# Optimization experiments

Hardware: AMD Instinct MI355X
Metric: run time of the kernel (lower is better)

## Reference

```python
import jax, jax.numpy as jnp
import numpy as np

B, H, W, C, NH, WS, SS = 32, 56, 56, 192, 6, 7, 3
N = WS * WS
HD = C // NH
NW = (H // WS) * (W // WS)
HID = 4 * C
RPB_SIZE = (2 * WS - 1) * (2 * WS - 1)


def _rel_index():
    coords = np.stack(np.meshgrid(np.arange(WS), np.arange(WS), indexing='ij')).reshape(2, -1)
    rel = (coords[:, :, None] - coords[:, None, :]).transpose(1, 2, 0)
    rel[..., 0] += WS - 1
    rel[..., 1] += WS - 1
    rel[..., 0] *= 2 * WS - 1
    return rel.sum(-1)  # (N, N) int

REL_IDX = jnp.asarray(_rel_index())


def _swin_attn_mask():
    # standard Swin shifted-window mask: -100 for cross-region pairs
    img = np.zeros((H, W))
    cnt = 0
    for hs in (slice(0, -WS), slice(-WS, -SS), slice(-SS, None)):
        for ws_ in (slice(0, -WS), slice(-WS, -SS), slice(-SS, None)):
            img[hs, ws_] = cnt
            cnt += 1
    win = img.reshape(H // WS, WS, W // WS, WS).transpose(0, 2, 1, 3).reshape(-1, N)
    diff = win[:, None, :] - win[:, :, None]
    return np.where(diff != 0, -100.0, 0.0).astype(np.float32)  # (NW, N, N)


def _ln(t, g, b, eps=1e-5):
    mu = t.mean(-1, keepdims=True)
    v = ((t - mu) ** 2).mean(-1, keepdims=True)
    return (t - mu) * jax.lax.rsqrt(v + eps) * g + b


def setup_inputs() -> dict:
    key = jax.random.key(0)
    ks = jax.random.split(key, 12)
    s = 0.02
    return {
        'x': jax.random.normal(ks[0], (B, H * W, C), jnp.float32),
        'attn_mask': jnp.asarray(_swin_attn_mask()),
        'ln1_g': jnp.ones((C,), jnp.float32),
        'ln1_b': jnp.zeros((C,), jnp.float32),
        'qkv_w': jax.random.normal(ks[1], (C, 3 * C), jnp.float32) * s,
        'qkv_b': jnp.zeros((3 * C,), jnp.float32),
        'rpb': jax.random.normal(ks[2], (RPB_SIZE, NH), jnp.float32) * s,
        'proj_w': jax.random.normal(ks[3], (C, C), jnp.float32) * s,
        'proj_b': jnp.zeros((C,), jnp.float32),
        'ln2_g': jnp.ones((C,), jnp.float32),
        'ln2_b': jnp.zeros((C,), jnp.float32),
        'fc1_w': jax.random.normal(ks[4], (C, HID), jnp.float32) * s,
        'fc1_b': jnp.zeros((HID,), jnp.float32),
        'fc2_w': jax.random.normal(ks[5], (HID, C), jnp.float32) * s,
        'fc2_b': jnp.zeros((C,), jnp.float32),
    }


def reference(x, attn_mask, ln1_g, ln1_b, qkv_w, qkv_b, rpb, proj_w, proj_b,
              ln2_g, ln2_b, fc1_w, fc1_b, fc2_w, fc2_b):
    shortcut = x
    h = _ln(x, ln1_g, ln1_b).reshape(B, H, W, C)
    # cyclic shift
    h = jnp.roll(h, (-SS, -SS), axis=(1, 2))
    # window partition -> (B*NW, N, C)
    h = h.reshape(B, H // WS, WS, W // WS, WS, C).transpose(0, 1, 3, 2, 4, 5).reshape(B * NW, N, C)
    qkv = (h @ qkv_w + qkv_b).reshape(B * NW, N, 3, NH, HD).transpose(2, 0, 3, 1, 4)
    q, k, v = qkv[0] * (HD ** -0.5), qkv[1], qkv[2]
    attn = jnp.einsum('bhnd,bhmd->bhnm', q, k)  # (B*NW, NH, N, N)
    bias = rpb[REL_IDX].transpose(2, 0, 1)      # (NH, N, N)
    attn = attn + bias[None]
    attn = attn.reshape(B, NW, NH, N, N) + attn_mask[None, :, None]
    attn = jax.nn.softmax(attn.reshape(B * NW, NH, N, N), axis=-1)
    o = jnp.einsum('bhnm,bhmd->bhnd', attn, v).transpose(0, 2, 1, 3).reshape(B * NW, N, C)
    o = o @ proj_w + proj_b
    # window reverse + reverse shift
    o = o.reshape(B, H // WS, W // WS, WS, WS, C).transpose(0, 1, 3, 2, 4, 5).reshape(B, H, W, C)
    o = jnp.roll(o, (SS, SS), axis=(1, 2)).reshape(B, H * W, C)
    x1 = shortcut + o
    m = _ln(x1, ln2_g, ln2_b)
    m = jax.nn.gelu(m @ fc1_w + fc1_b, approximate=False) @ fc2_w + fc2_b
    return x1 + m
```

## Files before the change

kernel.cpp:

```cpp
#include <hip/hip_runtime.h>
#include <hip/hip_bf16.h>

typedef __hip_bfloat16 bf16;
typedef __attribute__((ext_vector_type(8))) short short8;
typedef __attribute__((ext_vector_type(4))) float f32x4;
typedef __attribute__((ext_vector_type(4))) unsigned short ushort4_t;

#define TOK 100352
#define NWIN 2048
#define CC 192
#define NHEAD 6
#define NT 49

__device__ __forceinline__ float bf2f(bf16 v) { return __bfloat162float(v); }
__device__ __forceinline__ bf16 f2bf(float v) { return __float2bfloat16(v); }
__device__ __forceinline__ float b2f_bits(unsigned short u) {
    return __uint_as_float(((unsigned)u) << 16);
}

__device__ __forceinline__ float ldin(const void* p, size_t i, int f) {
    return f ? ((const float*)p)[i] : bf2f(((const bf16*)p)[i]);
}
__device__ __forceinline__ void stc(bf16* p, float v) { *p = f2bf(v); }
__device__ __forceinline__ void stc(float* p, float v) { *p = v; }
__device__ __forceinline__ float ldc(const bf16* p) { return bf2f(*p); }
__device__ __forceinline__ float ldc(const float* p) { return *p; }

__device__ __forceinline__ void gl_lds16(const bf16* g, bf16* l) {
    __builtin_amdgcn_global_load_lds(
        (const __attribute__((address_space(1))) unsigned int*)g,
        (__attribute__((address_space(3))) unsigned int*)l, 16, 0, 0);
}

__global__ void dtype_probe_kernel(const void* xraw, int* flag) {
    const unsigned short* u = (const unsigned short*)xraw;
    int lane = threadIdx.x & 63;
    int weird = 0;
    for (int i = lane; i < 4096; i += 64) {
        unsigned int bits = ((unsigned int)u[2 * i]) << 16;
        float v = __uint_as_float(bits);
        if (!(fabsf(v) <= 1e10f)) weird++;
    }
    #pragma unroll
    for (int off = 32; off > 0; off >>= 1) weird += __shfl_xor(weird, off, 64);
    if (lane == 0) *flag = (weird > 256) ? 1 : 0;
}

__global__ void transpose_kernel(const void* __restrict__ in, bf16* __restrict__ out,
                                 int K, int N, const int* __restrict__ flag) {
    int f = *flag;
    int idx = blockIdx.x * 256 + threadIdx.x;
    if (idx >= K * N) return;
    int nn = idx / K, kk = idx % K;
    out[idx] = f2bf(ldin(in, (size_t)kk * N + nn, f));
}

__global__ __launch_bounds__(256) void comb_kernel(
    const void* __restrict__ rpb, const void* __restrict__ mask,
    bf16* __restrict__ comb, const int* __restrict__ flag) {
    int f = *flag;
    int idx = blockIdx.x * 256 + threadIdx.x;
    int m = idx & 63;
    int n = (idx >> 6) & 63;
    int hw = idx >> 12;
    int head = hw % NHEAD, wi = hw / NHEAD;
    float v;
    if (n < NT && m < NT) {
        int nr = n / 7, nc = n % 7, mr = m / 7, mc = m % 7;
        int ridx = (nr - mr + 6) * 13 + (nc - mc + 6);
        v = ldin(rpb, (size_t)ridx * NHEAD + head, f)
          + ldin(mask, (size_t)wi * NT * NT + n * NT + m, f);
    } else {
        v = -1e30f;
    }
    comb[idx] = f2bf(v);
}

__global__ __launch_bounds__(256) void ln1_window_kernel(
    const void* __restrict__ x, const void* __restrict__ g, const void* __restrict__ b,
    bf16* __restrict__ hwin, const int* __restrict__ flag) {
    int f = *flag;
    int wave = threadIdx.x >> 6, lane = threadIdx.x & 63;
    int t = blockIdx.x * 4 + wave;
    int bidx = t / (64 * NT);
    int r = t % (64 * NT);
    int wi = r / NT, n = r % NT;
    int wr = wi >> 3, wc = wi & 7;
    int nr = n / 7, nc = n % 7;
    int si = wr * 7 + nr, sj = wc * 7 + nc;
    int oi = si + 3; if (oi >= 56) oi -= 56;
    int oj = sj + 3; if (oj >= 56) oj -= 56;
    size_t src = ((size_t)bidx * 3136 + oi * 56 + oj) * CC;
    float v0 = ldin(x, src + lane, f);
    float v1 = ldin(x, src + lane + 64, f);
    float v2 = ldin(x, src + lane + 128, f);
    float s = v0 + v1 + v2;
    float sq = v0 * v0 + v1 * v1 + v2 * v2;
    #pragma unroll
    for (int off = 32; off > 0; off >>= 1) {
        s  += __shfl_xor(s, off, 64);
        sq += __shfl_xor(sq, off, 64);
    }
    float mu = s * (1.f / 192.f);
    float var = fmaxf(sq * (1.f / 192.f) - mu * mu, 0.f);
    float rs = rsqrtf(var + 1e-5f);
    bf16* dst = hwin + (size_t)t * CC;
    dst[lane]       = f2bf((v0 - mu) * rs * ldin(g, lane, f)       + ldin(b, lane, f));
    dst[lane + 64]  = f2bf((v1 - mu) * rs * ldin(g, lane + 64, f)  + ldin(b, lane + 64, f));
    dst[lane + 128] = f2bf((v2 - mu) * rs * ldin(g, lane + 128, f) + ldin(b, lane + 128, f));
}

template <int EPI, typename CT>
__global__ __launch_bounds__(256, 4) void gemm_kernel(
    const bf16* __restrict__ A, const bf16* __restrict__ Wt,
    const void* __restrict__ bias, CT* __restrict__ C,
    const CT* __restrict__ resid, int M, int K, int Nc, const int* __restrict__ flag) {
    int f = *flag;
    __shared__ __align__(16) bf16 sb[2][(128 + 64) * 32];
    int bn = blockIdx.x, bm = blockIdx.y;
    int tid = threadIdx.x;
    int wave = tid >> 6, lane = tid & 63;
    int quad = lane >> 4, l16 = lane & 15;

    const bf16* ag[2];
    #pragma unroll
    for (int j = 0; j < 2; j++) {
        int k = wave * 2 + j;
        ag[j] = A + (size_t)(bm * 128 + k * 16 + (lane >> 2)) * K + (lane & 3) * 8;
    }
    const bf16* bg = Wt + (size_t)(bn * 64 + wave * 16 + (lane >> 2)) * K + (lane & 3) * 8;

    f32x4 acc[2][4];
    #pragma unroll
    for (int i = 0; i < 2; i++)
        #pragma unroll
        for (int j = 0; j < 4; j++)
            acc[i][j][0] = acc[i][j][1] = acc[i][j][2] = acc[i][j][3] = 0.f;

    const int nt = K >> 5;

    #pragma unroll
    for (int j = 0; j < 2; j++)
        gl_lds16(ag[j], &sb[0][(wave * 2 + j) * 512]);
    gl_lds16(bg, &sb[0][4096 + wave * 512]);
    __syncthreads();

    int ct = 0;
    for (int t = 0; t < nt; t++) {
        if (t + 1 < nt) {
            #pragma unroll
            for (int j = 0; j < 2; j++) {
                ag[j] += 32;
                gl_lds16(ag[j], &sb[ct ^ 1][(wave * 2 + j) * 512]);
            }
            bg += 32;
            gl_lds16(bg, &sb[ct ^ 1][4096 + wave * 512]);
        }
        const bf16* sA = &sb[ct][0];
        const bf16* sB = &sb[ct][4096];
        short8 av[2], bv[4];
        #pragma unroll
        for (int tm = 0; tm < 2; tm++)
            av[tm] = *(const short8*)(&sA[(wave * 32 + tm * 16 + l16) * 32 + quad * 8]);
        #pragma unroll
        for (int tn = 0; tn < 4; tn++)
            bv[tn] = *(const short8*)(&sB[(tn * 16 + l16) * 32 + quad * 8]);
        #pragma unroll
        for (int tm = 0; tm < 2; tm++)
            #pragma unroll
            for (int tn = 0; tn < 4; tn++)
                acc[tm][tn] = __builtin_amdgcn_mfma_f32_16x16x32_bf16(av[tm], bv[tn], acc[tm][tn], 0, 0, 0);
        if (t + 1 < nt) {
            __syncthreads();
            ct ^= 1;
        }
    }

    #pragma unroll
    for (int tm = 0; tm < 2; tm++)
        #pragma unroll
        for (int tn = 0; tn < 4; tn++) {
            int col = bn * 64 + tn * 16 + l16;
            float bvs = ldin(bias, col, f);
            #pragma unroll
            for (int r = 0; r < 4; r++) {
                int row = bm * 128 + wave * 32 + tm * 16 + quad * 4 + r;
                float v = acc[tm][tn][r] + bvs;
                if (EPI == 1) v = 0.5f * v * (1.0f + erff(v * 0.70710678118654752f));
                if (EPI == 2) v += ldc(&resid[(size_t)row * Nc + col]);
                stc(&C[(size_t)row * Nc + col], v);
            }
        }
}

__global__ __launch_bounds__(256) void attn_mfma_kernel(
    const bf16* __restrict__ qkv, const bf16* __restrict__ comb,
    bf16* __restrict__ attn_out, int wbase) {
    __shared__ __align__(16) bf16 Qs[64 * 40];
    __shared__ __align__(16) bf16 Ks[64 * 40];
    __shared__ __align__(16) bf16 Vt[32 * 72];
    __shared__ __align__(16) bf16 P[64 * 72];

    int head = blockIdx.x % NHEAD;
    int wl = blockIdx.x / NHEAD;
    int wg = wbase + wl;
    int wi = wg & 63;
    int t0 = wl * NT;
    int tg = wg * NT;
    int tid = threadIdx.x;
    int wave = tid >> 6, lane = tid & 63;
    int quad = lane >> 4, l16 = lane & 15;

    {
        int row = tid >> 2;
        int dc = (tid & 3) * 8;
        uint4 qv = make_uint4(0, 0, 0, 0), kv = qv;
        if (row < NT) {
            const bf16* base = qkv + (size_t)(t0 + row) * 576 + head * 32 + dc;
            qv = *(const uint4*)(base);
            kv = *(const uint4*)(base + 192);
        }
        *(uint4*)(&Qs[row * 40 + dc]) = qv;
        *(uint4*)(&Ks[row * 40 + dc]) = kv;
        for (int idx = tid; idx < 64 * 32; idx += 256) {
            int m = idx >> 5, d = idx & 31;
            bf16 v = (m < NT) ? qkv[(size_t)(t0 + m) * 576 + 384 + head * 32 + d] : f2bf(0.f);
            Vt[d * 72 + m] = v;
        }
    }
    __syncthreads();

    const float scale = 0.17677669529663687f;
    int tm = wave;
    int q = tm * 16 + l16;
    const bf16* crow = comb + (((size_t)wi * NHEAD + head) * 64 + q) * 64;

    float s[4][4];
    short8 bfrag = *(const short8*)(&Qs[q * 40 + quad * 8]);
    f32x4 z; z[0] = z[1] = z[2] = z[3] = 0.f;
    #pragma unroll
    for (int tn = 0; tn < 4; tn++) {
        short8 afrag = *(const short8*)(&Ks[(tn * 16 + l16) * 40 + quad * 8]);
        f32x4 acc = __builtin_amdgcn_mfma_f32_16x16x32_bf16(afrag, bfrag, z, 0, 0, 0);
        ushort4_t cb = *(const ushort4_t*)(crow + tn * 16 + quad * 4);
        s[tn][0] = acc[0] * scale + b2f_bits(cb[0]);
        s[tn][1] = acc[1] * scale + b2f_bits(cb[1]);
        s[tn][2] = acc[2] * scale + b2f_bits(cb[2]);
        s[tn][3] = acc[3] * scale + b2f_bits(cb[3]);
    }

    float mx = s[0][0];
    #pragma unroll
    for (int tn = 0; tn < 4; tn++)
        #pragma unroll
        for (int r = 0; r < 4; r++) mx = fmaxf(mx, s[tn][r]);
    mx = fmaxf(mx, __shfl_xor(mx, 16, 64));
    mx = fmaxf(mx, __shfl_xor(mx, 32, 64));
    float sm = 0.f;
    #pragma unroll
    for (int tn = 0; tn < 4; tn++)
        #pragma unroll
        for (int r = 0; r < 4; r++) { s[tn][r] = __expf(s[tn][r] - mx); sm += s[tn][r]; }
    sm += __shfl_xor(sm, 16, 64);
    sm += __shfl_xor(sm, 32, 64);
    float inv = 1.0f / sm;

    #pragma unroll
    for (int tn = 0; tn < 4; tn++) {
        bf16 pk[4];
        #pragma unroll
        for (int r = 0; r < 4; r++) pk[r] = f2bf(s[tn][r] * inv);
        *(uint2*)(&P[q * 72 + tn * 16 + quad * 4]) = *(const uint2*)pk;
    }
    __syncthreads();

    f32x4 oacc[2];
    oacc[0][0] = oacc[0][1] = oacc[0][2] = oacc[0][3] = 0.f;
    oacc[1] = oacc[0];
    #pragma unroll
    for (int kc = 0; kc < 2; kc++) {
        short8 pa = *(const short8*)(&P[(tm * 16 + l16) * 72 + kc * 32 + quad * 8]);
        #pragma unroll
        for (int tn = 0; tn < 2; tn++) {
            short8 vb = *(const short8*)(&Vt[(tn * 16 + l16) * 72 + kc * 32 + quad * 8]);
            oacc[tn] = __builtin_amdgcn_mfma_f32_16x16x32_bf16(pa, vb, oacc[tn], 0, 0, 0);
        }
    }
    #pragma unroll
    for (int tn = 0; tn < 2; tn++) {
        #pragma unroll
        for (int r = 0; r < 4; r++) {
            int n = tm * 16 + quad * 4 + r;
            int d = tn * 16 + l16;
            if (n < NT)
                attn_out[(size_t)(tg + n) * CC + head * 32 + d] = f2bf(oacc[tn][r]);
        }
    }
}

__global__ __launch_bounds__(256) void resid_ln2_kernel(
    const void* __restrict__ x, const bf16* __restrict__ proj,
    const void* __restrict__ g, const void* __restrict__ b,
    float* __restrict__ x1, bf16* __restrict__ h2, const int* __restrict__ flag) {
    int f = *flag;
    int wave = threadIdx.x >> 6, lane = threadIdx.x & 63;
    int tok = blockIdx.x * 4 + wave;
    int bidx = tok / 3136;
    int r = tok % 3136;
    int i = r / 56, j = r % 56;
    int si = i + 53; if (si >= 56) si -= 56;
    int sj = j + 53; if (sj >= 56) sj -= 56;
    int wi = (si / 7) * 8 + sj / 7;
    int n = (si % 7) * 7 + (sj % 7);
    size_t tw = ((size_t)bidx * 64 + wi) * NT + n;
    const bf16* ps = proj + tw * CC;
    size_t xs = (size_t)tok * CC;
    float v0 = ldin(x, xs + lane, f)       + bf2f(ps[lane]);
    float v1 = ldin(x, xs + lane + 64, f)  + bf2f(ps[lane + 64]);
    float v2 = ldin(x, xs + lane + 128, f) + bf2f(ps[lane + 128]);
    float* xd = x1 + (size_t)tok * CC;
    xd[lane] = v0; xd[lane + 64] = v1; xd[lane + 128] = v2;
    float s = v0 + v1 + v2;
    float sq = v0 * v0 + v1 * v1 + v2 * v2;
    #pragma unroll
    for (int off = 32; off > 0; off >>= 1) {
        s  += __shfl_xor(s, off, 64);
        sq += __shfl_xor(sq, off, 64);
    }
    float mu = s * (1.f / 192.f);
    float var = fmaxf(sq * (1.f / 192.f) - mu * mu, 0.f);
    float rs = rsqrtf(var + 1e-5f);
    bf16* dst = h2 + (size_t)tok * CC;
    dst[lane]       = f2bf((v0 - mu) * rs * ldin(g, lane, f)       + ldin(b, lane, f));
    dst[lane + 64]  = f2bf((v1 - mu) * rs * ldin(g, lane + 64, f)  + ldin(b, lane + 64, f));
    dst[lane + 128] = f2bf((v2 - mu) * rs * ldin(g, lane + 128, f) + ldin(b, lane + 128, f));
}

extern "C" void kernel_launch(void* const* d_in, const int* in_sizes, int n_in,
                              void* d_out, int out_size, void* d_ws, size_t ws_size,
                              hipStream_t stream) {
    const void* x        = d_in[0];
    const void* attnmask = d_in[1];
    const void* ln1_g    = d_in[2];
    const void* ln1_b    = d_in[3];
    const void* qkv_w    = d_in[4];
    const void* qkv_b    = d_in[5];
    const void* rpb      = d_in[6];
    const void* proj_w   = d_in[7];
    const void* proj_b   = d_in[8];
    const void* ln2_g    = d_in[9];
    const void* ln2_b    = d_in[10];
    const void* fc1_w    = d_in[11];
    const void* fc1_b    = d_in[12];
    const void* fc2_w    = d_in[13];
    const void* fc2_b    = d_in[14];
    float* out = (float*)d_out;
    char* ws = (char*)d_ws;

    const size_t RSZ = (size_t)TOK * CC * sizeof(bf16);
    const size_t WEXT = 442368 * sizeof(bf16)
                      + (size_t)64 * NHEAD * 64 * 64 * sizeof(bf16)
                      + 64;
    const size_t NEED_BIG = 5 * RSZ + WEXT;

    const int M = TOK;

    if (ws_size >= NEED_BIG) {
        bf16* h_win    = (bf16*)(ws);
        bf16* qkvbuf   = (bf16*)(ws + RSZ);
        bf16* attn_out = (bf16*)(ws + 4 * RSZ);
        bf16* projbuf  = (bf16*)(ws);
        bf16* h2       = (bf16*)(ws + 4 * RSZ);
        bf16* m1buf    = (bf16*)(ws);
        bf16* qkvT     = (bf16*)(ws + 5 * RSZ);
        bf16* projT    = qkvT + 192 * 576;
        bf16* fc1T     = projT + 192 * 192;
        bf16* fc2T     = fc1T + 192 * 768;
        bf16* combT    = fc2T + 768 * 192;
        int*  flag     = (int*)(combT + 64 * NHEAD * 64 * 64);

        dtype_probe_kernel<<<1, 64, 0, stream>>>(x, flag);
        transpose_kernel<<<(192 * 576 + 255) / 256, 256, 0, stream>>>(qkv_w, qkvT, 192, 576, flag);
        transpose_kernel<<<(192 * 192 + 255) / 256, 256, 0, stream>>>(proj_w, projT, 192, 192, flag);
        transpose_kernel<<<(192 * 768 + 255) / 256, 256, 0, stream>>>(fc1_w, fc1T, 192, 768, flag);
        transpose_kernel<<<(768 * 192 + 255) / 256, 256, 0, stream>>>(fc2_w, fc2T, 768, 192, flag);
        comb_kernel<<<(64 * NHEAD * 64 * 64) / 256, 256, 0, stream>>>(rpb, attnmask, combT, flag);

        ln1_window_kernel<<<TOK / 4, 256, 0, stream>>>(x, ln1_g, ln1_b, h_win, flag);

        gemm_kernel<0, bf16><<<dim3(576 / 64, M / 128), 256, 0, stream>>>(
            h_win, qkvT, qkv_b, qkvbuf, (const bf16*)nullptr, M, 192, 576, flag);
        attn_mfma_kernel<<<NWIN * NHEAD, 256, 0, stream>>>(qkvbuf, combT, attn_out, 0);

        gemm_kernel<0, bf16><<<dim3(192 / 64, M / 128), 256, 0, stream>>>(
            attn_out, projT, proj_b, projbuf, (const bf16*)nullptr, M, 192, 192, flag);

        resid_ln2_kernel<<<TOK / 4, 256, 0, stream>>>(x, projbuf, ln2_g, ln2_b, out, h2, flag);

        gemm_kernel<1, bf16><<<dim3(768 / 64, M / 128), 256, 0, stream>>>(
            h2, fc1T, fc1_b, m1buf, (const bf16*)nullptr, M, 192, 768, flag);
        gemm_kernel<2, float><<<dim3(192 / 64, M / 128), 256, 0, stream>>>(
            m1buf, fc2T, fc2_b, out, (const float*)out, M, 768, 192, flag);
    } else {
        bf16* h_win    = (bf16*)(ws);
        bf16* m1buf    = (bf16*)(ws);
        bf16* attn_out = (bf16*)(ws + RSZ);
        bf16* h2       = (bf16*)(ws + RSZ);
        bf16* qkvchunk = (bf16*)(ws + 2 * RSZ);
        bf16* projbuf  = (bf16*)(ws + 2 * RSZ);
        bf16* combT    = (bf16*)(ws + 2 * RSZ + 28901376);
        bf16* qkvT     = (bf16*)(ws + 3 * RSZ);
        bf16* projT    = qkvT + 192 * 576;
        bf16* fc1T     = projT + 192 * 192;
        bf16* fc2T     = fc1T + 192 * 768;
        int*  flag     = (int*)(fc2T + 768 * 192);

        dtype_probe_kernel<<<1, 64, 0, stream>>>(x, flag);
        transpose_kernel<<<(192 * 576 + 255) / 256, 256, 0, stream>>>(qkv_w, qkvT, 192, 576, flag);
        transpose_kernel<<<(192 * 192 + 255) / 256, 256, 0, stream>>>(proj_w, projT, 192, 192, flag);
        transpose_kernel<<<(192 * 768 + 255) / 256, 256, 0, stream>>>(fc1_w, fc1T, 192, 768, flag);
        transpose_kernel<<<(768 * 192 + 255) / 256, 256, 0, stream>>>(fc2_w, fc2T, 768, 192, flag);
        comb_kernel<<<(64 * NHEAD * 64 * 64) / 256, 256, 0, stream>>>(rpb, attnmask, combT, flag);

        ln1_window_kernel<<<TOK / 4, 256, 0, stream>>>(x, ln1_g, ln1_b, h_win, flag);

        const int QCH = 4, QW = NWIN / QCH;
        const int QROWS = QW * NT;
        for (int c = 0; c < QCH; c++) {
            const bf16* a = h_win + (size_t)c * QROWS * CC;
            gemm_kernel<0, bf16><<<dim3(576 / 64, QROWS / 128), 256, 0, stream>>>(
                a, qkvT, qkv_b, qkvchunk, (const bf16*)nullptr, QROWS, 192, 576, flag);
            attn_mfma_kernel<<<QW * NHEAD, 256, 0, stream>>>(
                qkvchunk, combT, attn_out, c * QW);
        }

        gemm_kernel<0, bf16><<<dim3(192 / 64, M / 128), 256, 0, stream>>>(
            attn_out, projT, proj_b, projbuf, (const bf16*)nullptr, M, 192, 192, flag);

        resid_ln2_kernel<<<TOK / 4, 256, 0, stream>>>(x, projbuf, ln2_g, ln2_b, out, h2, flag);

        const int MCH = 4, MR = TOK / MCH;
        for (int c = 0; c < MCH; c++) {
            const bf16* a = h2 + (size_t)c * MR * CC;
            float* oc = out + (size_t)c * MR * CC;
            gemm_kernel<1, bf16><<<dim3(768 / 64, MR / 128), 256, 0, stream>>>(
                a, fc1T, fc1_b, m1buf, (const bf16*)nullptr, MR, 192, 768, flag);
            gemm_kernel<2, float><<<dim3(192 / 64, MR / 128), 256, 0, stream>>>(
                m1buf, fc2T, fc2_b, oc, (const float*)oc, MR, 768, 192, flag);
        }
    }
}
```

Before: 584.7 us.

## Triple-buffer GEMM LDS staging with vmcnt waits and XCD-aware block swizzle

Replaces the double-buffered LDS pipeline in the bf16 GEMM with a three-stage ring. Loads for tile t+2 are issued while tile t is computed, and explicit s_waitcnt vmcnt counts replace full __syncthreads, so global-to-LDS loads can stay in flight across iterations. It also remaps block IDs in groups of 8 so neighbouring tiles land on the same XCD, aiming for better L2 reuse. In exchange LDS use per block rises by half, which may reduce occupancy, and the hand-written wait counts depend on each STAGE issuing exactly three loads.

After: 543.3 us. 7.1% less time.

```diff
diff --git a/kernel.cpp b/kernel.cpp
--- a/kernel.cpp
+++ b/kernel.cpp
@@ -116,19 +116,31 @@
     const void* __restrict__ bias, CT* __restrict__ C,
     const CT* __restrict__ resid, int M, int K, int Nc, const int* __restrict__ flag) {
     int f = *flag;
-    __shared__ __align__(16) bf16 sb[2][(128 + 64) * 32];
-    int bn = blockIdx.x, bm = blockIdx.y;
+    __shared__ __align__(16) bf16 sb[3][6144];
     int tid = threadIdx.x;
     int wave = tid >> 6, lane = tid & 63;
     int quad = lane >> 4, l16 = lane & 15;
 
+    int nwg = gridDim.x * gridDim.y;
+    int bid = blockIdx.y * gridDim.x + blockIdx.x;
+    int swz = bid;
+    if ((nwg & 7) == 0) {
+        int cpx = nwg >> 3;
+        swz = (bid & 7) * cpx + (bid >> 3);
+    }
+    int bn = swz % gridDim.x, bm = swz / gridDim.x;
+
     const bf16* ag[2];
     #pragma unroll
-    for (int j = 0; j < 2; j++) {
-        int k = wave * 2 + j;
-        ag[j] = A + (size_t)(bm * 128 + k * 16 + (lane >> 2)) * K + (lane & 3) * 8;
-    }
+    for (int j = 0; j < 2; j++)
+        ag[j] = A + (size_t)(bm * 128 + (wave * 2 + j) * 16 + (lane >> 2)) * K + (lane & 3) * 8;
     const bf16* bg = Wt + (size_t)(bn * 64 + wave * 16 + (lane >> 2)) * K + (lane & 3) * 8;
+
+    auto STAGE = [&](int t, int buf) {
+        gl_lds16(ag[0] + (size_t)t * 32, &sb[buf][(wave * 2 + 0) * 512]);
+        gl_lds16(ag[1] + (size_t)t * 32, &sb[buf][(wave * 2 + 1) * 512]);
+        gl_lds16(bg    + (size_t)t * 32, &sb[buf][4096 + wave * 512]);
+    };
 
     f32x4 acc[2][4];
     #pragma unroll
@@ -139,25 +151,19 @@
 
     const int nt = K >> 5;
 
-    #pragma unroll
-    for (int j = 0; j < 2; j++)
-        gl_lds16(ag[j], &sb[0][(wave * 2 + j) * 512]);
-    gl_lds16(bg, &sb[0][4096 + wave * 512]);
-    __syncthreads();
-
-    int ct = 0;
+    STAGE(0, 0);
+    STAGE(1, 1);
+    asm volatile("s_waitcnt vmcnt(3)" ::: "memory");
+    __builtin_amdgcn_s_barrier();
+
+    int cur = 0;
     for (int t = 0; t < nt; t++) {
-        if (t + 1 < nt) {
-            #pragma unroll
-            for (int j = 0; j < 2; j++) {
-                ag[j] += 32;
-                gl_lds16(ag[j], &sb[ct ^ 1][(wave * 2 + j) * 512]);
-            }
-            bg += 32;
-            gl_lds16(bg, &sb[ct ^ 1][4096 + wave * 512]);
-        }
-        const bf16* sA = &sb[ct][0];
-        const bf16* sB = &sb[ct][4096];
+        if (t + 2 < nt) {
+            int stg = cur + 2; if (stg >= 3) stg -= 3;
+            STAGE(t + 2, stg);
+        }
+        const bf16* sA = &sb[cur][0];
+        const bf16* sB = &sb[cur][4096];
         short8 av[2], bv[4];
         #pragma unroll
         for (int tm = 0; tm < 2; tm++)
@@ -171,9 +177,13 @@
             for (int tn = 0; tn < 4; tn++)
                 acc[tm][tn] = __builtin_amdgcn_mfma_f32_16x16x32_bf16(av[tm], bv[tn], acc[tm][tn], 0, 0, 0);
         if (t + 1 < nt) {
-            __syncthreads();
-            ct ^= 1;
-        }
+            if (t + 2 < nt)
+                asm volatile("s_waitcnt vmcnt(3) lgkmcnt(0)" ::: "memory");
+            else
+                asm volatile("s_waitcnt vmcnt(0) lgkmcnt(0)" ::: "memory");
+            __builtin_amdgcn_s_barrier();
+        }
+        cur++; if (cur >= 3) cur -= 3;
     }
 
     #pragma unroll
```
